# Kernel tuning notes

Hardware: AMD Instinct MI355X
Metric: run time of the kernel (lower is better)

Reference implementation:

```python
import jax, jax.numpy as jnp
import numpy as np

B, D, L, H = 8, 512, 2048, 8
DH = D // H
NEG = -1e30


def setup_inputs() -> dict:
    key = jax.random.key(0)
    k1, k2, k3, k4 = jax.random.split(key, 4)
    queries = jax.random.normal(k1, (B, D, L), dtype=jnp.float32)
    mask = jax.random.randint(k2, (B, L), 0, 2, dtype=jnp.int32)
    w_mem = jax.random.normal(k3, (2 * D, D), dtype=jnp.float32) * (1.0 / np.sqrt(D))
    w_q = jax.random.normal(k4, (D, D), dtype=jnp.float32) * (1.0 / np.sqrt(D))
    return {"queries": queries, "mask": mask, "w_mem": w_mem, "w_q": w_q}


def reference(queries, mask, w_mem, w_q):
    # 1x1 conv == pointwise GEMM over channel dim. queries: [B, D, L]
    memory = jnp.einsum('od,bdl->blo', w_mem, queries)  # [B, L, 2D]
    query = jnp.einsum('od,bdl->blo', w_q, queries)     # [B, L, D]

    def split_heads(x):  # [B, L, C] -> [B, H, L, C/H]
        b, l, c = x.shape
        return x.reshape(b, l, H, c // H).transpose(0, 2, 1, 3)

    k, v = memory[..., :D], memory[..., D:]
    Q = split_heads(query) * (DH ** -0.5)  # [B, H, L, DH]
    K = split_heads(k)
    V = split_heads(v)

    logits = jnp.einsum('bhqd,bhkd->bhqk', Q, K)  # [B, H, L, L]
    m = mask.astype(jnp.float32)[:, None, None, :]  # [B, 1, 1, L]
    logits = logits * m + (1.0 - m) * NEG
    weights = jax.nn.softmax(logits, axis=-1)
    x = jnp.einsum('bhqk,bhkd->bhqd', weights, V)  # [B, H, L, DH]
    # combine heads -> [B, L, D] -> transpose back to [B, D, L]
    out = x.transpose(0, 2, 1, 3).reshape(B, L, D).transpose(0, 2, 1)
    return out
```

## Files before the change

kernel.cpp:

```cpp
#include <hip/hip_runtime.h>
#include <hip/hip_bf16.h>

#define NB 8
#define ND 512
#define NL 2048
#define NH 8
#define NDH 64
#define VROWS 72

typedef __attribute__((ext_vector_type(8))) short bf16x8;
typedef __attribute__((ext_vector_type(4))) float f32x4;
typedef __attribute__((ext_vector_type(4))) unsigned int u32x4;

__device__ __forceinline__ unsigned short f2bf(float x) {
    return (unsigned short)((__float_as_uint(x) + 0x8000u) >> 16);
}

__device__ __forceinline__ float exp2_fast(float x) {
#if __has_builtin(__builtin_amdgcn_exp2f)
    return __builtin_amdgcn_exp2f(x);
#else
    return exp2f(x);
#endif
}

__device__ __forceinline__ unsigned int pack_bf16(float a, float b) {
#if __has_builtin(__builtin_amdgcn_cvt_pk_bf16_f32)
    auto r = __builtin_amdgcn_cvt_pk_bf16_f32(a, b);
    unsigned int u;
    __builtin_memcpy(&u, &r, 4);
    return u;
#else
    unsigned int ua = __float_as_uint(a) + 0x8000u;
    unsigned int ub = __float_as_uint(b) + 0x8000u;
    return __builtin_amdgcn_perm(ub, ua, 0x07060302u);
#endif
}

__device__ __forceinline__ int perm64(int k) {
    return (k & 32) | ((k & 12) << 1) | ((k & 16) >> 2) | (k & 3);
}

__device__ __forceinline__ void async16(void* lds, const void* g) {
    __builtin_amdgcn_global_load_lds(
        (const __attribute__((address_space(1))) unsigned int*)g,
        (__attribute__((address_space(3))) unsigned int*)lds, 16, 0, 0);
}

__global__ __launch_bounds__(256) void prep(
    const float* __restrict__ qin,
    const float* __restrict__ w_mem, const float* __restrict__ w_q,
    const int* __restrict__ maskp,
    unsigned short* __restrict__ Xt, unsigned short* __restrict__ Wc,
    unsigned short* __restrict__ Vt, unsigned short* __restrict__ Kh,
    int* __restrict__ cmap, int* __restrict__ ntile, int* __restrict__ nvalid)
{
    const int bid = blockIdx.x;
    const int t = threadIdx.x;
    if (bid < 2048) {
        __shared__ __align__(16) unsigned short T[64][72];
        const int l0 = (bid & 31) * 64, d0 = ((bid >> 5) & 7) * 64, b = bid >> 8;
        const float* X = qin + ((size_t)b * ND + d0) * NL + l0;
        #pragma unroll
        for (int i = 0; i < 4; ++i) {
            int e = t + i * 256;
            int d = e >> 4, l4 = (e & 15) * 4;
            float4 v = *(const float4*)(X + (size_t)d * NL + l4);
            T[l4 + 0][d] = f2bf(v.x);
            T[l4 + 1][d] = f2bf(v.y);
            T[l4 + 2][d] = f2bf(v.z);
            T[l4 + 3][d] = f2bf(v.w);
        }
        __syncthreads();
        #pragma unroll
        for (int i = 0; i < 2; ++i) {
            int e = t + i * 256;
            int row = e >> 3, c8 = (e & 7) * 8;
            *(bf16x8*)(Xt + ((size_t)b * NL + l0 + row) * ND + d0 + c8) =
                *(const bf16x8*)&T[row][c8];
        }
    } else if (bid < 2432) {
        int idx = ((bid - 2048) * 256 + t) * 8;
        int o = idx >> 9, k = idx & 511;
        const float* src;
        float sc;
        if (o < 1024) { src = w_mem + (size_t)o * ND + k; sc = 1.0f; }
        else          { src = w_q + (size_t)(o - 1024) * ND + k;
                        sc = 0.125f * 1.4426950408889634f; }
        float4 f0 = *(const float4*)src;
        float4 f1 = *(const float4*)(src + 4);
        ushort4 p0 = { f2bf(f0.x * sc), f2bf(f0.y * sc), f2bf(f0.z * sc), f2bf(f0.w * sc) };
        ushort4 p1 = { f2bf(f1.x * sc), f2bf(f1.y * sc), f2bf(f1.z * sc), f2bf(f1.w * sc) };
        *(ushort4*)(Wc + idx) = p0;
        *(ushort4*)(Wc + idx + 4) = p1;
    } else {
        __shared__ int wsum[4];
        const int sb = bid - 2432;
        const int b = sb >> 3, hh = sb & 7;
        const int lane = t & 63, wv = t >> 6;
        int4 ma = *(const int4*)&maskp[b * NL + t * 8];
        int4 mb = *(const int4*)&maskp[b * NL + t * 8 + 4];
        int m[8] = {ma.x, ma.y, ma.z, ma.w, mb.x, mb.y, mb.z, mb.w};
        int loc = 0;
        #pragma unroll
        for (int i = 0; i < 8; ++i) loc += m[i];
        int sc = loc;
        #pragma unroll
        for (int off = 1; off < 64; off <<= 1) {
            int v = __shfl_up(sc, off);
            if (lane >= off) sc += v;
        }
        if (lane == 63) wsum[wv] = sc;
        __syncthreads();
        int wbase = 0;
        #pragma unroll
        for (int i = 0; i < 4; ++i) if (i < wv) wbase += wsum[i];
        int j = wbase + sc - loc;
        if (hh == 0) {
            int jj = j;
            #pragma unroll
            for (int i = 0; i < 8; ++i) {
                cmap[b * NL + t * 8 + i] = m[i] ? jj : -1;
                jj += m[i];
            }
        }
        const int nb = wsum[0] + wsum[1] + wsum[2] + wsum[3];
        const int Nt = (nb + 63) & ~63;
        if (hh == 0 && t == 0) { ntile[b] = Nt >> 6; nvalid[b] = nb; }
        const int pad = Nt - nb;
        for (int e = t; e < pad * 64; e += 256) {
            int jj = nb + (e >> 6), dd = e & 63;
            int slot = (jj & ~63) | perm64(jj & 63);
            Vt[(((size_t)(b * NH + hh)) * VROWS + dd) * NL + slot] = 0;
            Kh[(((size_t)(b * NH + hh)) * NL + jj) * NDH + dd] = 0;
        }
    }
}

__global__ __launch_bounds__(256, 3) void proj_mfma(
    const unsigned short* __restrict__ Wc,
    const unsigned short* __restrict__ Xt,
    const int* __restrict__ cmap,
    unsigned short* __restrict__ Kh,
    unsigned short* __restrict__ Qh,
    unsigned short* __restrict__ Vt)
{
    __shared__ __align__(16) unsigned short As[128 * 64];
    __shared__ __align__(16) unsigned short Bs[128 * 64];

    const int b  = blockIdx.z;
    const int m0 = blockIdx.y * 128;
    const int n0 = blockIdx.x * 128;
    const int t  = threadIdx.x;
    const int w = t >> 6, lane = t & 63, quad = lane >> 4, lq = lane & 15;
    const int wo = (w >> 1) * 64, wl = (w & 1) * 64;
    const int lr = lane >> 3;
    const int cbsw = (lane & 7) ^ lr;
    const bool isV = (m0 >= 512) && (m0 < 1024);
    const f32x4 z4 = {0.f, 0.f, 0.f, 0.f};
    const int sw[2] = {(quad ^ (lq & 7)) * 8, ((4 + quad) ^ (lq & 7)) * 8};

    f32x4 acc[4][4];
    #pragma unroll
    for (int im = 0; im < 4; ++im)
        #pragma unroll
        for (int in = 0; in < 4; ++in) acc[im][in] = z4;

    if (!isV) {
        for (int k0 = 0; k0 < ND; k0 += 64) {
            __syncthreads();
            #pragma unroll 2
            for (int i = w; i < 32; i += 4) {
                if (i < 16) {
                    int R = i * 8;
                    async16(&As[R * 64],
                            Wc + (size_t)(m0 + R + lr) * ND + k0 + cbsw * 8);
                } else {
                    int R = (i - 16) * 8;
                    async16(&Bs[R * 64],
                            Xt + ((size_t)b * NL + n0 + R + lr) * ND + k0 + cbsw * 8);
                }
            }
            __syncthreads();
            #pragma unroll
            for (int ks = 0; ks < 2; ++ks) {
                bf16x8 af[4], bfr[4];
                #pragma unroll
                for (int im = 0; im < 4; ++im)
                    af[im] = *(const bf16x8*)&As[(wo + im * 16 + lq) * 64 + sw[ks]];
                #pragma unroll
                for (int in = 0; in < 4; ++in)
                    bfr[in] = *(const bf16x8*)&Bs[(wl + in * 16 + lq) * 64 + sw[ks]];
                #pragma unroll
                for (int im = 0; im < 4; ++im)
                    #pragma unroll
                    for (int in = 0; in < 4; ++in)
                        acc[im][in] = __builtin_amdgcn_mfma_f32_16x16x32_bf16(
                            af[im], bfr[in], acc[im][in], 0, 0, 0);
            }
        }
        if (m0 < 512) {
            int j[4];
            #pragma unroll
            for (int in = 0; in < 4; ++in)
                j[in] = cmap[b * NL + n0 + wl + in * 16 + lq];
            #pragma unroll
            for (int im = 0; im < 4; ++im) {
                int o  = (m0 + wo + im * 16 + quad * 4) & 511;
                int hh = o >> 6, dh = o & 63;
                #pragma unroll
                for (int in = 0; in < 4; ++in) {
                    if (j[in] >= 0) {
                        ushort4 pk = { f2bf(acc[im][in][0]), f2bf(acc[im][in][1]),
                                       f2bf(acc[im][in][2]), f2bf(acc[im][in][3]) };
                        *(ushort4*)&Kh[(((size_t)b * NH + hh) * NL + j[in]) * NDH + dh] = pk;
                    }
                }
            }
        } else {
            #pragma unroll
            for (int im = 0; im < 4; ++im) {
                int o  = (m0 + wo + im * 16 + quad * 4) & 511;
                int hh = o >> 6, dh = o & 63;
                #pragma unroll
                for (int in = 0; in < 4; ++in) {
                    int l = n0 + wl + in * 16 + lq;
                    ushort4 pk = { f2bf(acc[im][in][0]), f2bf(acc[im][in][1]),
                                   f2bf(acc[im][in][2]), f2bf(acc[im][in][3]) };
                    *(ushort4*)&Qh[(((size_t)b * NH + hh) * NL + l) * NDH + dh] = pk;
                }
            }
        }
    } else {
        for (int k0 = 0; k0 < ND; k0 += 64) {
            __syncthreads();
            #pragma unroll 2
            for (int i = w; i < 32; i += 4) {
                if (i < 16) {
                    int R = i * 8;
                    async16(&As[R * 64],
                            Wc + (size_t)(m0 + R + lr) * ND + k0 + cbsw * 8);
                } else {
                    int R = (i - 16) * 8;
                    async16(&Bs[R * 64],
                            Xt + ((size_t)b * NL + n0 + R + lr) * ND + k0 + cbsw * 8);
                }
            }
            __syncthreads();
            #pragma unroll
            for (int ks = 0; ks < 2; ++ks) {
                bf16x8 af[4], bfr[4];
                #pragma unroll
                for (int im = 0; im < 4; ++im)
                    af[im] = *(const bf16x8*)&As[(wo + im * 16 + lq) * 64 + sw[ks]];
                #pragma unroll
                for (int in = 0; in < 4; ++in)
                    bfr[in] = *(const bf16x8*)&Bs[(wl + in * 16 + lq) * 64 + sw[ks]];
                #pragma unroll
                for (int im = 0; im < 4; ++im)
                    #pragma unroll
                    for (int in = 0; in < 4; ++in)
                        acc[im][in] = __builtin_amdgcn_mfma_f32_16x16x32_bf16(
                            bfr[im], af[in], acc[im][in], 0, 0, 0);
            }
        }
        #pragma unroll
        for (int im = 0; im < 4; ++im) {
            int l4 = n0 + wl + im * 16 + quad * 4;
            int4 j4 = *(const int4*)&cmap[b * NL + l4];
            int jj[4] = {j4.x, j4.y, j4.z, j4.w};
            int slot[4];
            #pragma unroll
            for (int r = 0; r < 4; ++r)
                slot[r] = (jj[r] & ~63) | perm64(jj[r] & 63);
            #pragma unroll
            for (int in = 0; in < 4; ++in) {
                int o  = m0 - 512 + wo + in * 16 + lq;
                int hh = o >> 6, dd = o & 63;
                const size_t rowbase = (((size_t)(b * NH + hh)) * VROWS + dd) * NL;
                #pragma unroll
                for (int r = 0; r < 4; ++r)
                    if (jj[r] >= 0)
                        Vt[rowbase + slot[r]] = f2bf(acc[im][in][r]);
            }
        }
    }
}

__global__ __launch_bounds__(512, 4) void attn_mfma(
    const unsigned short* __restrict__ Qh,
    const unsigned short* __restrict__ Kh,
    const unsigned short* __restrict__ Vt,
    const int* __restrict__ ntilep,
    const int* __restrict__ nvalidp,
    float* __restrict__ out)
{
    __shared__ __align__(16) unsigned short Ks2[2][2 * 64 * 64];
    __shared__ __align__(16) unsigned short Vs2[2][2 * 64 * 64];

    const int id = blockIdx.x;
    const int h  = id & 7;
    const int b  = (id >> 3) & 7;
    const int q0 = (id >> 6) * 256;
    const int t = threadIdx.x;
    const int w = t >> 6;
    const int lane = t & 63, quad = lane >> 4, lq = lane & 15;
    const int lr = lane >> 3;
    const int cbsw = (lane & 7) ^ lr;
    const f32x4 z4 = {0.f, 0.f, 0.f, 0.f};

    const unsigned short* Qg = Qh + ((size_t)(b * NH + h)) * NL * NDH;
    const unsigned short* Kg = Kh + ((size_t)(b * NH + h)) * NL * NDH;
    const unsigned short* Vg = Vt + ((size_t)(b * NH + h)) * VROWS * NL;
    const int ntiles = ntilep[b];

    const int sw0 = (quad ^ (lq & 7)) * 8;
    const int sw1 = ((4 + quad) ^ (lq & 7)) * 8;

    const unsigned short* kgp = Kg + (size_t)(w * 8 + lr) * NDH + cbsw * 8;
    const unsigned short* vgp = Vg + (size_t)(w * 8 + lr) * NL + cbsw * 8;

    auto stage128 = [&](unsigned short* Kd, unsigned short* Vd, int kn) {
        async16(Kd + w * 512,        kgp + (size_t)kn * NDH);
        async16(Kd + 4096 + w * 512, kgp + (size_t)(kn + 64) * NDH);
        async16(Vd + w * 512,        vgp + kn);
        async16(Vd + 4096 + w * 512, vgp + kn + 64);
    };

    stage128(Ks2[0], Vs2[0], 0);

    bf16x8 qf[2][2];
    #pragma unroll
    for (int ni = 0; ni < 2; ++ni)
        #pragma unroll
        for (int ks = 0; ks < 2; ++ks)
            qf[ni][ks] = *(const bf16x8*)
                &Qg[(size_t)(q0 + w * 32 + ni * 16 + lq) * NDH + ks * 32 + quad * 8];

    f32x4 oacc[4][2];
    #pragma unroll
    for (int dm = 0; dm < 4; ++dm)
        #pragma unroll
        for (int ni = 0; ni < 2; ++ni) oacc[dm][ni] = z4;
    float ls[2] = {0.f, 0.f};

    auto sub = [&](const unsigned short* KsB, const unsigned short* VsB) {
        const unsigned short* kb0 = KsB + lq * 64 + sw0;
        const unsigned short* kb1 = KsB + lq * 64 + sw1;
        const unsigned short* vb0 = VsB + lq * 64 + sw0;
        const unsigned short* vb1 = VsB + lq * 64 + sw1;

        f32x4 sacc[4][2];
        #pragma unroll
        for (int mi = 0; mi < 4; ++mi) {
            bf16x8 kf = *(const bf16x8*)&kb0[mi * 1024];
            sacc[mi][0] = __builtin_amdgcn_mfma_f32_16x16x32_bf16(kf, qf[0][0], z4, 0, 0, 0);
            sacc[mi][1] = __builtin_amdgcn_mfma_f32_16x16x32_bf16(kf, qf[1][0], z4, 0, 0, 0);
        }
        #pragma unroll
        for (int mi = 0; mi < 4; ++mi) {
            bf16x8 kf = *(const bf16x8*)&kb1[mi * 1024];
            sacc[mi][0] = __builtin_amdgcn_mfma_f32_16x16x32_bf16(kf, qf[0][1], sacc[mi][0], 0, 0, 0);
            sacc[mi][1] = __builtin_amdgcn_mfma_f32_16x16x32_bf16(kf, qf[1][1], sacc[mi][1], 0, 0, 0);
        }

        #pragma unroll
        for (int ks = 0; ks < 2; ++ks) {
            u32x4 pfu[2];
            #pragma unroll
            for (int half = 0; half < 2; ++half) {
                const int mi = ks * 2 + half, jp = half * 2;
                #pragma unroll
                for (int ni = 0; ni < 2; ++ni) {
                    float e0 = exp2_fast(sacc[mi][ni][0]);
                    float e1 = exp2_fast(sacc[mi][ni][1]);
                    float e2 = exp2_fast(sacc[mi][ni][2]);
                    float e3 = exp2_fast(sacc[mi][ni][3]);
                    ls[ni] += (e0 + e1) + (e2 + e3);
                    pfu[ni][jp + 0] = pack_bf16(e0, e1);
                    pfu[ni][jp + 1] = pack_bf16(e2, e3);
                }
            }
            const unsigned short* vb = ks ? vb1 : vb0;
            #pragma unroll
            for (int dm = 0; dm < 4; ++dm) {
                bf16x8 vf = *(const bf16x8*)&vb[dm * 1024];
                oacc[dm][0] = __builtin_amdgcn_mfma_f32_16x16x32_bf16(
                    vf, __builtin_bit_cast(bf16x8, pfu[0]), oacc[dm][0], 0, 0, 0);
                oacc[dm][1] = __builtin_amdgcn_mfma_f32_16x16x32_bf16(
                    vf, __builtin_bit_cast(bf16x8, pfu[1]), oacc[dm][1], 0, 0, 0);
            }
        }
    };

    const int npairs = ntiles >> 1, odd = ntiles & 1;
    int p = 0;
    #pragma unroll 1
    for (; p + 1 < npairs; ++p) {
        const int cb = p & 1;
        __syncthreads();
        stage128(Ks2[cb ^ 1], Vs2[cb ^ 1], (p + 1) * 128);
        sub(Ks2[cb], Vs2[cb]);
        sub(Ks2[cb] + 4096, Vs2[cb] + 4096);
    }
    if (npairs > 0) {
        const int cb = p & 1;
        __syncthreads();
        if (odd) stage128(Ks2[cb ^ 1], Vs2[cb ^ 1], npairs * 128);
        sub(Ks2[cb], Vs2[cb]);
        sub(Ks2[cb] + 4096, Vs2[cb] + 4096);
        ++p;
    }
    if (odd) {
        const int cb = p & 1;
        __syncthreads();
        sub(Ks2[cb], Vs2[cb]);
    }

    const float padc = (float)(ntiles * 64 - nvalidp[b]);
    float inv[2];
    #pragma unroll
    for (int ni = 0; ni < 2; ++ni) {
        float s = ls[ni];
        s += __shfl_xor(s, 16);
        s += __shfl_xor(s, 32);
        inv[ni] = 1.0f / (s - padc);
    }

    #pragma unroll
    for (int dm = 0; dm < 4; ++dm)
        #pragma unroll
        for (int ni = 0; ni < 2; ++ni)
            #pragma unroll
            for (int r = 0; r < 4; ++r) {
                int dh = dm * 16 + quad * 4 + r;
                int l  = q0 + w * 32 + ni * 16 + lq;
                out[((size_t)b * ND + h * NDH + dh) * NL + l] =
                    oacc[dm][ni][r] * inv[ni];
            }
}

extern "C" void kernel_launch(void* const* d_in, const int* in_sizes, int n_in,
                              void* d_out, int out_size, void* d_ws, size_t ws_size,
                              hipStream_t stream) {
    const float* queries = (const float*)d_in[0];
    const int*   maskp   = (const int*)d_in[1];
    const float* w_mem   = (const float*)d_in[2];
    const float* w_q     = (const float*)d_in[3];
    float* out = (float*)d_out;

    const size_t headElems  = (size_t)NB * NH * NL * NDH;
    const size_t vElems     = (size_t)NB * NH * VROWS * NL;
    unsigned short* Kh = (unsigned short*)d_ws;
    unsigned short* Vt = Kh + headElems;
    unsigned short* Qh = Vt + vElems;
    unsigned short* Wc = Qh + headElems;
    unsigned short* Xt = Wc + (size_t)1536 * ND;
    int* cmap   = (int*)(Xt + (size_t)NB * NL * ND);
    int* ntile  = cmap + NB * NL;
    int* nvalid = ntile + NB;

    prep<<<2496, 256, 0, stream>>>(queries, w_mem, w_q, maskp,
                                   Xt, Wc, Vt, Kh, cmap, ntile, nvalid);

    dim3 g1(NL / 128, 1536 / 128, NB);
    proj_mfma<<<g1, 256, 0, stream>>>(Wc, Xt, cmap, Kh, Qh, Vt);

    attn_mfma<<<512, 512, 0, stream>>>(Qh, Kh, Vt, ntile, nvalid, out);
}
```

Baseline: 171.6 us.

## Give each attention wave 64 query rows with 4 waves per block

The attention kernel moves from 512 threads (8 waves, 32 query rows each) to 256 threads (4 waves, 64 query rows each), keeping the 256-row block tile. Each K/V fragment read from shared memory now feeds twice as many MFMAs, which cuts LDS read traffic per FLOP. Each thread issues twice as many async staging copies. The QK^T computation is also restructured per key half so fewer score accumulators are live at once. The cost is more accumulator registers per thread and fewer waves per block to hide latency.

```diff
diff --git a/kernel.cpp b/kernel.cpp
--- a/kernel.cpp
+++ b/kernel.cpp
@@ -287,7 +287,7 @@
     }
 }
 
-__global__ __launch_bounds__(512, 4) void attn_mfma(
+__global__ __launch_bounds__(256, 2) void attn_mfma(
     const unsigned short* __restrict__ Qh,
     const unsigned short* __restrict__ Kh,
     const unsigned short* __restrict__ Vt,
@@ -317,32 +317,38 @@
     const int sw0 = (quad ^ (lq & 7)) * 8;
     const int sw1 = ((4 + quad) ^ (lq & 7)) * 8;
 
-    const unsigned short* kgp = Kg + (size_t)(w * 8 + lr) * NDH + cbsw * 8;
-    const unsigned short* vgp = Vg + (size_t)(w * 8 + lr) * NL + cbsw * 8;
+    const unsigned short* kgp  = Kg + (size_t)(w * 16 + lr) * NDH + cbsw * 8;
+    const unsigned short* kgp8 = kgp + (size_t)8 * NDH;
+    const unsigned short* vgp  = Vg + (size_t)(w * 16 + lr) * NL + cbsw * 8;
+    const unsigned short* vgp8 = vgp + (size_t)8 * NL;
 
     auto stage128 = [&](unsigned short* Kd, unsigned short* Vd, int kn) {
-        async16(Kd + w * 512,        kgp + (size_t)kn * NDH);
-        async16(Kd + 4096 + w * 512, kgp + (size_t)(kn + 64) * NDH);
-        async16(Vd + w * 512,        vgp + kn);
-        async16(Vd + 4096 + w * 512, vgp + kn + 64);
+        async16(Kd + w * 1024,              kgp  + (size_t)kn * NDH);
+        async16(Kd + w * 1024 + 512,        kgp8 + (size_t)kn * NDH);
+        async16(Kd + 4096 + w * 1024,       kgp  + (size_t)(kn + 64) * NDH);
+        async16(Kd + 4096 + w * 1024 + 512, kgp8 + (size_t)(kn + 64) * NDH);
+        async16(Vd + w * 1024,              vgp  + kn);
+        async16(Vd + w * 1024 + 512,        vgp8 + kn);
+        async16(Vd + 4096 + w * 1024,       vgp  + kn + 64);
+        async16(Vd + 4096 + w * 1024 + 512, vgp8 + kn + 64);
     };
 
     stage128(Ks2[0], Vs2[0], 0);
 
-    bf16x8 qf[2][2];
+    bf16x8 qf[4][2];
     #pragma unroll
-    for (int ni = 0; ni < 2; ++ni)
+    for (int ni = 0; ni < 4; ++ni)
         #pragma unroll
         for (int ks = 0; ks < 2; ++ks)
             qf[ni][ks] = *(const bf16x8*)
-                &Qg[(size_t)(q0 + w * 32 + ni * 16 + lq) * NDH + ks * 32 + quad * 8];
-
-    f32x4 oacc[4][2];
+                &Qg[(size_t)(q0 + w * 64 + ni * 16 + lq) * NDH + ks * 32 + quad * 8];
+
+    f32x4 oacc[4][4];
     #pragma unroll
     for (int dm = 0; dm < 4; ++dm)
         #pragma unroll
-        for (int ni = 0; ni < 2; ++ni) oacc[dm][ni] = z4;
-    float ls[2] = {0.f, 0.f};
+        for (int ni = 0; ni < 4; ++ni) oacc[dm][ni] = z4;
+    float ls[4] = {0.f, 0.f, 0.f, 0.f};
 
     auto sub = [&](const unsigned short* KsB, const unsigned short* VsB) {
         const unsigned short* kb0 = KsB + lq * 64 + sw0;
@@ -350,32 +356,33 @@
         const unsigned short* vb0 = VsB + lq * 64 + sw0;
         const unsigned short* vb1 = VsB + lq * 64 + sw1;
 
-        f32x4 sacc[4][2];
-        #pragma unroll
-        for (int mi = 0; mi < 4; ++mi) {
-            bf16x8 kf = *(const bf16x8*)&kb0[mi * 1024];
-            sacc[mi][0] = __builtin_amdgcn_mfma_f32_16x16x32_bf16(kf, qf[0][0], z4, 0, 0, 0);
-            sacc[mi][1] = __builtin_amdgcn_mfma_f32_16x16x32_bf16(kf, qf[1][0], z4, 0, 0, 0);
-        }
-        #pragma unroll
-        for (int mi = 0; mi < 4; ++mi) {
-            bf16x8 kf = *(const bf16x8*)&kb1[mi * 1024];
-            sacc[mi][0] = __builtin_amdgcn_mfma_f32_16x16x32_bf16(kf, qf[0][1], sacc[mi][0], 0, 0, 0);
-            sacc[mi][1] = __builtin_amdgcn_mfma_f32_16x16x32_bf16(kf, qf[1][1], sacc[mi][1], 0, 0, 0);
-        }
-
         #pragma unroll
         for (int ks = 0; ks < 2; ++ks) {
-            u32x4 pfu[2];
+            f32x4 sacc[2][4];
             #pragma unroll
             for (int half = 0; half < 2; ++half) {
-                const int mi = ks * 2 + half, jp = half * 2;
-                #pragma unroll
-                for (int ni = 0; ni < 2; ++ni) {
-                    float e0 = exp2_fast(sacc[mi][ni][0]);
-                    float e1 = exp2_fast(sacc[mi][ni][1]);
-                    float e2 = exp2_fast(sacc[mi][ni][2]);
-                    float e3 = exp2_fast(sacc[mi][ni][3]);
+                const int mi = ks * 2 + half;
+                bf16x8 kf0 = *(const bf16x8*)&kb0[mi * 1024];
+                #pragma unroll
+                for (int ni = 0; ni < 4; ++ni)
+                    sacc[half][ni] = __builtin_amdgcn_mfma_f32_16x16x32_bf16(
+                        kf0, qf[ni][0], z4, 0, 0, 0);
+                bf16x8 kf1 = *(const bf16x8*)&kb1[mi * 1024];
+                #pragma unroll
+                for (int ni = 0; ni < 4; ++ni)
+                    sacc[half][ni] = __builtin_amdgcn_mfma_f32_16x16x32_bf16(
+                        kf1, qf[ni][1], sacc[half][ni], 0, 0, 0);
+            }
+            u32x4 pfu[4];
+            #pragma unroll
+            for (int half = 0; half < 2; ++half) {
+                const int jp = half * 2;
+                #pragma unroll
+                for (int ni = 0; ni < 4; ++ni) {
+                    float e0 = exp2_fast(sacc[half][ni][0]);
+                    float e1 = exp2_fast(sacc[half][ni][1]);
+                    float e2 = exp2_fast(sacc[half][ni][2]);
+                    float e3 = exp2_fast(sacc[half][ni][3]);
                     ls[ni] += (e0 + e1) + (e2 + e3);
                     pfu[ni][jp + 0] = pack_bf16(e0, e1);
                     pfu[ni][jp + 1] = pack_bf16(e2, e3);
@@ -385,10 +392,10 @@
             #pragma unroll
             for (int dm = 0; dm < 4; ++dm) {
                 bf16x8 vf = *(const bf16x8*)&vb[dm * 1024];
-                oacc[dm][0] = __builtin_amdgcn_mfma_f32_16x16x32_bf16(
-                    vf, __builtin_bit_cast(bf16x8, pfu[0]), oacc[dm][0], 0, 0, 0);
-                oacc[dm][1] = __builtin_amdgcn_mfma_f32_16x16x32_bf16(
-                    vf, __builtin_bit_cast(bf16x8, pfu[1]), oacc[dm][1], 0, 0, 0);
+                #pragma unroll
+                for (int ni = 0; ni < 4; ++ni)
+                    oacc[dm][ni] = __builtin_amdgcn_mfma_f32_16x16x32_bf16(
+                        vf, __builtin_bit_cast(bf16x8, pfu[ni]), oacc[dm][ni], 0, 0, 0);
             }
         }
     };
@@ -418,9 +425,9 @@
     }
 
     const float padc = (float)(ntiles * 64 - nvalidp[b]);
-    float inv[2];
+    float inv[4];
     #pragma unroll
-    for (int ni = 0; ni < 2; ++ni) {
+    for (int ni = 0; ni < 4; ++ni) {
         float s = ls[ni];
         s += __shfl_xor(s, 16);
         s += __shfl_xor(s, 32);
@@ -430,11 +437,11 @@
     #pragma unroll
     for (int dm = 0; dm < 4; ++dm)
         #pragma unroll
-        for (int ni = 0; ni < 2; ++ni)
+        for (int ni = 0; ni < 4; ++ni)
             #pragma unroll
             for (int r = 0; r < 4; ++r) {
                 int dh = dm * 16 + quad * 4 + r;
-                int l  = q0 + w * 32 + ni * 16 + lq;
+                int l  = q0 + w * 64 + ni * 16 + lq;
                 out[((size_t)b * ND + h * NDH + dh) * NL + l] =
                     oacc[dm][ni][r] * inv[ni];
             }
@@ -466,5 +473,5 @@
     dim3 g1(NL / 128, 1536 / 128, NB);
     proj_mfma<<<g1, 256, 0, stream>>>(Wc, Xt, cmap, Kh, Qh, Vt);
 
-    attn_mfma<<<512, 512, 0, stream>>>(Qh, Kh, Vt, ntile, nvalid, out);
-}
+    attn_mfma<<<512, 256, 0, stream>>>(Qh, Kh, Vt, ntile, nvalid, out);
+}
```

Result: no change. 172.3 us (+0.4%).
